# Kernel optimization log

Measured on AMD Instinct MI355X. Metric: run time of the kernel, lower is better.

Reference implementation:

```python
import jax, jax.numpy as jnp
import numpy as np

C_V, C_F, C_D = 10, 64, 16
COSTS = jnp.array([10.0, 5.0, 2.0], dtype=jnp.float32)  # bandwidth cost per granularity
PENALTY = 0.0  # no_transmission_utility_penalty


def setup_inputs() -> dict:
    key = jax.random.key(0)
    k1, k2 = jax.random.split(key)
    B, H, W = 4, 192, 192
    collab = jax.random.normal(k1, (B, C_V + C_F + C_D, H, W), dtype=jnp.float32)
    utility = jax.random.normal(k2, (B, H, W, 3), dtype=jnp.float32)
    return {"collab_bev_data_list": collab, "utility_map_list": utility,
            "bandwidth_budget": 200000}


def _selection_mechanism(utility, budget_per_sample):
    # utility: [B, H, W, G]; returns [B, H, W] float selected granularity (-1 = none)
    B, H, W, G = utility.shape
    best_u = jnp.max(utility, axis=3)                      # [B,H,W]
    best_g = jnp.argmax(utility, axis=3)                   # [B,H,W]
    N = B * H * W
    flat_u = best_u.reshape(N)
    flat_g = best_g.reshape(N)
    b_idx = jnp.repeat(jnp.arange(B, dtype=jnp.int32), H * W)
    valid = flat_u > PENALTY
    cost = COSTS[flat_g]                                   # [N]
    # sort candidates by utility, descending (stable, matching list.sort)
    order = jnp.argsort(-flat_u)
    v_s = valid[order]
    c_s = cost[order]
    b_s = b_idx[order]

    # greedy budget-constrained selection per sample (sequential knapsack)
    def step(usage, item):
        v, c, b = item
        ok = v & (usage[b] + c <= budget_per_sample)
        usage = usage.at[b].add(jnp.where(ok, c, jnp.float32(0)))
        return usage, ok

    _, sel_sorted = jax.lax.scan(step, jnp.zeros((B,), jnp.float32), (v_s, c_s, b_s))
    selected = jnp.zeros((N,), bool).at[order].set(sel_sorted)
    idx = jnp.where(selected, flat_g.astype(jnp.float32), jnp.float32(-1.0))
    return idx.reshape(B, H, W)


def _build_sparse_bev(sel_idx, vox, feat, det):
    m0 = (sel_idx == 0.0)[:, None, :, :]
    m1 = (sel_idx == 1.0)[:, None, :, :]
    m2 = (sel_idx == 2.0)[:, None, :, :]
    return jnp.concatenate([vox * m0, feat * m1, det * m2], axis=1)


def reference(collab_bev_data_list, utility_map_list, bandwidth_budget):
    cav_num = collab_bev_data_list.shape[0]
    budget_per_sample = jnp.float32(bandwidth_budget / cav_num)
    sel_idx = _selection_mechanism(utility_map_list, budget_per_sample)
    vox = collab_bev_data_list[:, :C_V]
    feat = collab_bev_data_list[:, C_V:C_V + C_F]
    det = collab_bev_data_list[:, C_V + C_F:C_V + C_F + C_D]
    sparse = _build_sparse_bev(sel_idx, vox, feat, det)
    return sparse, sel_idx
```

## Files before the change

kernel.cpp:

```cpp
#include <hip/hip_runtime.h>
#include <stdint.h>
#include <math.h>

#define B_    4
#define H_    192
#define W_    192
#define HW    (H_*W_)
#define NPIX  (B_*HW)
#define C_V   10
#define C_F   64
#define C_D   16
#define C_ALL (C_V+C_F+C_D)
#define NBINS 65536
#define CAP   3072

#define OFF_HIST   0u
#define OFF_COUNT  (4u*NBINS*4u)
#define OFF_SELX   (OFF_COUNT + 64u)
#define ZERO_BYTES (OFF_SELX + (uint32_t)NPIX)
#define OFF_KEY    ZERO_BYTES
#define OFF_G      (OFF_KEY + (uint32_t)NPIX*4u)
#define OFF_RES    (OFF_G + (uint32_t)NPIX)
#define OFF_LIST   (OFF_RES + 64u)

__device__ __forceinline__ uint32_t costOf(uint32_t g) {
    return g == 0u ? 10u : (g == 1u ? 5u : 2u);
}

__device__ __forceinline__ uint32_t budgetInt(const int* bptr) {
    double bps = (double)bptr[0] / (double)B_;
    float f = (float)bps;
    return (uint32_t)floorf(f);
}

__global__ void k_prep(const float* __restrict__ util, uint32_t* __restrict__ key,
                       uint8_t* __restrict__ gArr, uint32_t* __restrict__ hist) {
    int i = blockIdx.x * blockDim.x + threadIdx.x;
    if (i >= NPIX) return;
    const float* u = util + (size_t)i * 3;
    float u0 = u[0], u1 = u[1], u2 = u[2];
    float best = u0; uint32_t g = 0;
    if (u1 > best) { best = u1; g = 1; }
    if (u2 > best) { best = u2; g = 2; }
    uint32_t k = 0u;
    if (best > 0.0f) k = __float_as_uint(best) | 0x80000000u;
    key[i] = k;
    gArr[i] = (uint8_t)g;
    if (k) {
        int b = i / HW;
        atomicAdd(&hist[(size_t)b * NBINS + (k >> 16)], costOf(g));
    }
}

__global__ __launch_bounds__(1024) void k_cutoff(const uint32_t* __restrict__ hist,
                                                 const int* __restrict__ budget_ptr,
                                                 uint32_t* __restrict__ res) {
    int b = blockIdx.x;
    uint32_t budget = budgetInt(budget_ptr);
    __shared__ uint32_t scan[1024];
    __shared__ uint32_t f_bstar, f_usage;
    if (threadIdx.x == 0) { f_bstar = 0xFFFFFFFFu; f_usage = 0u; }
    int t = threadIdx.x;
    const uint32_t* hb = hist + (size_t)b * NBINS;
    int hi = 65535 - 64 * t;
    uint32_t cs = 0;
    for (int j = 0; j < 64; ++j) cs += hb[hi - j];
    scan[t] = cs;
    __syncthreads();
    for (int off = 1; off < 1024; off <<= 1) {
        uint32_t v = (t >= off) ? scan[t - off] : 0u;
        __syncthreads();
        scan[t] += v;
        __syncthreads();
    }
    uint32_t incl = scan[t], excl = incl - cs;
    if (excl <= budget && incl > budget) {
        uint32_t cum = excl;
        for (int j = 0; j < 64; ++j) {
            uint32_t hv = hb[hi - j];
            if (cum + hv > budget) { f_bstar = (uint32_t)(hi - j); f_usage = cum; break; }
            cum += hv;
        }
    }
    __syncthreads();
    if (threadIdx.x == 0) {
        uint32_t bs = f_bstar;
        res[b]     = bs;
        res[4 + b] = f_usage;
        uint32_t hl;
        if (bs == 0xFFFFFFFFu)      hl = 1u;
        else if (bs >= 0xFFFFu)     hl = 0xFFFFFFFFu;
        else                        hl = (bs + 1u) << 16;
        res[8 + b] = hl;
    }
}

__global__ void k_collect(const uint32_t* __restrict__ key, const uint8_t* __restrict__ gArr,
                          const uint32_t* __restrict__ res, uint32_t* __restrict__ count,
                          uint64_t* __restrict__ list) {
    int i = blockIdx.x * blockDim.x + threadIdx.x;
    if (i >= NPIX) return;
    uint32_t k = key[i];
    if (!k) return;
    int b = i / HW;
    if ((k >> 16) != res[b]) return;
    uint32_t idx = atomicAdd(&count[b], 1u);
    if (idx < CAP) {
        uint32_t pix = (uint32_t)(i - b * HW);
        uint64_t e = ((uint64_t)(~k) << 32) | ((uint64_t)pix << 2) | (uint64_t)gArr[i];
        list[(size_t)b * CAP + idx] = e;
    }
}

__global__ __launch_bounds__(512) void k_scan(const uint32_t* __restrict__ key,
                                              const uint8_t* __restrict__ gArr,
                                              const uint32_t* __restrict__ res,
                                              const uint32_t* __restrict__ count,
                                              const uint64_t* __restrict__ list,
                                              const int* __restrict__ budget_ptr,
                                              uint8_t* __restrict__ selx) {
    int b = blockIdx.x;
    uint32_t bstar = res[b];
    if (bstar == 0xFFFFFFFFu) return;
    uint32_t budget = budgetInt(budget_ptr);

    __shared__ uint64_t e[CAP];
    __shared__ uint64_t s[CAP];
    __shared__ uint64_t red[512];
    __shared__ uint32_t sh_r, sh_poskey, sh_pospix;

    uint32_t cnt = count[b];
    int n = (int)(cnt < (uint32_t)CAP ? cnt : (uint32_t)CAP);
    const uint64_t* lb = list + (size_t)b * CAP;
    for (int i = threadIdx.x; i < n; i += blockDim.x) e[i] = lb[i];
    __syncthreads();
    for (int i = threadIdx.x; i < n; i += blockDim.x) {
        uint64_t ei = e[i];
        int rk = 0;
        for (int j = 0; j < n; ++j) rk += (e[j] < ei);
        s[rk] = ei;
    }
    __syncthreads();
    if (threadIdx.x == 0) {
        uint32_t usage = res[4 + b];
        uint8_t* sx = selx + (size_t)b * HW;
        for (int i = 0; i < n; ++i) {
            uint64_t ei = s[i];
            uint32_t g = (uint32_t)(ei & 3u);
            uint32_t c = costOf(g);
            if (usage + c <= budget) { usage += c; sx[(ei >> 2) & 0xFFFFu] = 1; }
        }
        sh_r = budget - usage;
        sh_poskey = bstar << 16;
        sh_pospix = 0xFFFFFFFFu;
    }
    __syncthreads();

    const uint32_t* kb = key + (size_t)b * HW;
    const uint8_t*  gb = gArr + (size_t)b * HW;
    for (int round = 0; round < 8; ++round) {
        uint32_t r = sh_r;
        if (r < 2u) break;
        uint32_t pkey = sh_poskey, ppix = sh_pospix;
        uint64_t best = 0;
        for (int i = threadIdx.x; i < HW; i += blockDim.x) {
            uint32_t k = kb[i];
            if (!k) continue;
            if (!(k < pkey || (k == pkey && (uint32_t)i > ppix))) continue;
            if (costOf(gb[i]) > r) continue;
            uint64_t m = ((uint64_t)k << 16) | (uint64_t)(65535u - (uint32_t)i);
            if (m > best) best = m;
        }
        red[threadIdx.x] = best;
        __syncthreads();
        for (int off = 256; off > 0; off >>= 1) {
            if ((int)threadIdx.x < off) {
                uint64_t o = red[threadIdx.x + off];
                if (o > red[threadIdx.x]) red[threadIdx.x] = o;
            }
            __syncthreads();
        }
        if (threadIdx.x == 0) {
            uint64_t m = red[0];
            if (m == 0) sh_r = 0;
            else {
                uint32_t pix = 65535u - (uint32_t)(m & 0xFFFFu);
                uint32_t k   = (uint32_t)(m >> 16);
                uint32_t c   = costOf(gb[pix]);
                selx[(size_t)b * HW + pix] = 1;
                sh_r -= c;
                sh_poskey = k; sh_pospix = pix;
            }
        }
        __syncthreads();
    }
}

__global__ void k_selidx(const uint32_t* __restrict__ key, const uint8_t* __restrict__ gArr,
                         const uint8_t* __restrict__ selx, const uint32_t* __restrict__ res,
                         float* __restrict__ selOut) {
    int i = blockIdx.x * blockDim.x + threadIdx.x;
    if (i >= NPIX) return;
    int b = i / HW;
    uint32_t k = key[i];
    bool sel = (k != 0u && k >= res[8 + b]) || (selx[i] != 0);
    selOut[i] = sel ? (float)gArr[i] : -1.0f;
}

__global__ void k_sparse(const float* __restrict__ collab, const float* __restrict__ selOut,
                         float* __restrict__ out) {
    int tid = blockIdx.x * blockDim.x + threadIdx.x;
    int c = blockIdx.y, b = blockIdx.z;
    if (tid >= HW / 4) return;
    float want = (c < C_V) ? 0.0f : ((c < C_V + C_F) ? 1.0f : 2.0f);
    size_t po = (size_t)b * HW + (size_t)tid * 4;
    float4 s4 = *(const float4*)(selOut + po);
    size_t co = ((size_t)(b * C_ALL + c)) * HW + (size_t)tid * 4;
    float4 v = *(const float4*)(collab + co);
    float4 o;
    o.x = (s4.x == want) ? v.x : 0.0f;
    o.y = (s4.y == want) ? v.y : 0.0f;
    o.z = (s4.z == want) ? v.z : 0.0f;
    o.w = (s4.w == want) ? v.w : 0.0f;
    *(float4*)(out + co) = o;
}

extern "C" void kernel_launch(void* const* d_in, const int* in_sizes, int n_in,
                              void* d_out, int out_size, void* d_ws, size_t ws_size,
                              hipStream_t stream) {
    (void)in_sizes; (void)n_in; (void)out_size; (void)ws_size;
    const float* collab = (const float*)d_in[0];
    const float* util   = (const float*)d_in[1];
    const int*   budget = (const int*)d_in[2];

    uint8_t*  ws    = (uint8_t*)d_ws;
    uint32_t* hist  = (uint32_t*)(ws + OFF_HIST);
    uint32_t* count = (uint32_t*)(ws + OFF_COUNT);
    uint8_t*  selx  = ws + OFF_SELX;
    uint32_t* key   = (uint32_t*)(ws + OFF_KEY);
    uint8_t*  g     = ws + OFF_G;
    uint32_t* res   = (uint32_t*)(ws + OFF_RES);
    uint64_t* list  = (uint64_t*)(ws + OFF_LIST);

    float* outSparse = (float*)d_out;
    float* outSel    = outSparse + (size_t)B_ * C_ALL * HW;

    hipMemsetAsync(d_ws, 0, ZERO_BYTES, stream);

    k_prep   <<<(NPIX + 255) / 256, 256, 0, stream>>>(util, key, g, hist);
    k_cutoff <<<B_, 1024, 0, stream>>>(hist, budget, res);
    k_collect<<<(NPIX + 255) / 256, 256, 0, stream>>>(key, g, res, count, list);
    k_scan   <<<B_, 512, 0, stream>>>(key, g, res, count, list, budget, selx);
    k_selidx <<<(NPIX + 255) / 256, 256, 0, stream>>>(key, g, selx, res, outSel);
    dim3 grid6(HW / 4 / 256, C_ALL, B_);
    k_sparse <<<grid6, 256, 0, stream>>>(collab, outSel, outSparse);
}
```

Before: 86.68 us.

## Fuse selection pipeline into fewer kernels and halve histogram size

Cuts the launch chain from six kernels plus a memset down to four. Cutoff, collect and scan are merged into a single per-sample k_select block that gathers boundary-bin candidates into shared memory. The selection-index computation moves into k_sparse, and k_prep now handles four pixels per thread with vectorized loads and stores. Because only positive keys reach the histogram, it uses 32768 bins instead of 65536, which shrinks zeroing and the prefix scan. The risks are a smaller candidate cap (2048), a full-image rescan inside the single block, and extra key/g/selx loads repeated across all 90 channels in k_sparse.

```diff
diff --git a/kernel.cpp b/kernel.cpp
--- a/kernel.cpp
+++ b/kernel.cpp
@@ -11,17 +11,14 @@
 #define C_F   64
 #define C_D   16
 #define C_ALL (C_V+C_F+C_D)
-#define NBINS 65536
-#define CAP   3072
-
-#define OFF_HIST   0u
-#define OFF_COUNT  (4u*NBINS*4u)
-#define OFF_SELX   (OFF_COUNT + 64u)
-#define ZERO_BYTES (OFF_SELX + (uint32_t)NPIX)
-#define OFF_KEY    ZERO_BYTES
-#define OFF_G      (OFF_KEY + (uint32_t)NPIX*4u)
-#define OFF_RES    (OFF_G + (uint32_t)NPIX)
-#define OFF_LIST   (OFF_RES + 64u)
+#define HBINS 32768
+#define CAP   2048
+
+#define OFF_HIST 0u
+#define OFF_KEY  (4u*HBINS*4u)
+#define OFF_G    (OFF_KEY + (uint32_t)NPIX*4u)
+#define OFF_SELX (OFF_G + (uint32_t)NPIX)
+#define OFF_HL   (OFF_SELX + (uint32_t)NPIX)
 
 __device__ __forceinline__ uint32_t costOf(uint32_t g) {
     return g == 0u ? 10u : (g == 1u ? 5u : 2u);
@@ -33,38 +30,64 @@
     return (uint32_t)floorf(f);
 }
 
-__global__ void k_prep(const float* __restrict__ util, uint32_t* __restrict__ key,
-                       uint8_t* __restrict__ gArr, uint32_t* __restrict__ hist) {
+__global__ void k_zero(uint4* __restrict__ hist4) {
     int i = blockIdx.x * blockDim.x + threadIdx.x;
-    if (i >= NPIX) return;
-    const float* u = util + (size_t)i * 3;
-    float u0 = u[0], u1 = u[1], u2 = u[2];
-    float best = u0; uint32_t g = 0;
-    if (u1 > best) { best = u1; g = 1; }
-    if (u2 > best) { best = u2; g = 2; }
-    uint32_t k = 0u;
-    if (best > 0.0f) k = __float_as_uint(best) | 0x80000000u;
-    key[i] = k;
-    gArr[i] = (uint8_t)g;
-    if (k) {
-        int b = i / HW;
-        atomicAdd(&hist[(size_t)b * NBINS + (k >> 16)], costOf(g));
-    }
-}
-
-__global__ __launch_bounds__(1024) void k_cutoff(const uint32_t* __restrict__ hist,
+    hist4[i] = make_uint4(0u, 0u, 0u, 0u);
+}
+
+__global__ void k_prep(const float* __restrict__ util, uint4* __restrict__ key4,
+                       uint32_t* __restrict__ g4, uint32_t* __restrict__ selx4,
+                       uint32_t* __restrict__ hist) {
+    int t = blockIdx.x * blockDim.x + threadIdx.x;
+    if (t >= NPIX / 4) return;
+    const float4* u4 = (const float4*)util + (size_t)t * 3;
+    float4 a = u4[0], b4 = u4[1], c4 = u4[2];
+    float u[4][3] = { {a.x, a.y, a.z}, {a.w, b4.x, b4.y},
+                      {b4.z, b4.w, c4.x}, {c4.y, c4.z, c4.w} };
+    uint32_t kk[4]; uint32_t gpack = 0;
+    #pragma unroll
+    for (int p = 0; p < 4; ++p) {
+        float best = u[p][0]; uint32_t g = 0;
+        if (u[p][1] > best) { best = u[p][1]; g = 1; }
+        if (u[p][2] > best) { best = u[p][2]; g = 2; }
+        kk[p] = (best > 0.0f) ? (__float_as_uint(best) | 0x80000000u) : 0u;
+        gpack |= g << (8 * p);
+    }
+    key4[t] = make_uint4(kk[0], kk[1], kk[2], kk[3]);
+    g4[t] = gpack;
+    selx4[t] = 0u;
+    int b = (t * 4) / HW;
+    #pragma unroll
+    for (int p = 0; p < 4; ++p)
+        if (kk[p])
+            atomicAdd(&hist[(size_t)b * HBINS + ((kk[p] >> 16) & 32767u)],
+                      costOf((gpack >> (8 * p)) & 3u));
+}
+
+__global__ __launch_bounds__(1024) void k_select(const uint32_t* __restrict__ key,
+                                                 const uint8_t* __restrict__ g,
+                                                 const uint32_t* __restrict__ hist,
                                                  const int* __restrict__ budget_ptr,
-                                                 uint32_t* __restrict__ res) {
+                                                 uint8_t* __restrict__ selx,
+                                                 uint32_t* __restrict__ hl_out) {
     int b = blockIdx.x;
+    int t = threadIdx.x;
     uint32_t budget = budgetInt(budget_ptr);
+
     __shared__ uint32_t scan[1024];
-    __shared__ uint32_t f_bstar, f_usage;
-    if (threadIdx.x == 0) { f_bstar = 0xFFFFFFFFu; f_usage = 0u; }
-    int t = threadIdx.x;
-    const uint32_t* hb = hist + (size_t)b * NBINS;
-    int hi = 65535 - 64 * t;
+    __shared__ uint64_t e[CAP];
+    __shared__ uint64_t s[CAP];
+    __shared__ uint64_t red[1024];
+    __shared__ uint32_t f_b2, f_usage, sh_n, sh_r, sh_poskey, sh_pospix;
+
+    if (t == 0) { f_b2 = 0xFFFFFFFFu; f_usage = 0u; sh_n = 0u; }
+    __syncthreads();
+
+    const uint32_t* hb = hist + (size_t)b * HBINS;
+    int hi = 32767 - 32 * t;
     uint32_t cs = 0;
-    for (int j = 0; j < 64; ++j) cs += hb[hi - j];
+    #pragma unroll 4
+    for (int j = 0; j < 32; ++j) cs += hb[hi - j];
     scan[t] = cs;
     __syncthreads();
     for (int off = 1; off < 1024; off <<= 1) {
@@ -76,94 +99,66 @@
     uint32_t incl = scan[t], excl = incl - cs;
     if (excl <= budget && incl > budget) {
         uint32_t cum = excl;
-        for (int j = 0; j < 64; ++j) {
+        for (int j = 0; j < 32; ++j) {
             uint32_t hv = hb[hi - j];
-            if (cum + hv > budget) { f_bstar = (uint32_t)(hi - j); f_usage = cum; break; }
+            if (cum + hv > budget) { f_b2 = (uint32_t)(hi - j); f_usage = cum; break; }
             cum += hv;
         }
     }
     __syncthreads();
-    if (threadIdx.x == 0) {
-        uint32_t bs = f_bstar;
-        res[b]     = bs;
-        res[4 + b] = f_usage;
+    uint32_t b2 = f_b2;
+    if (t == 0) {
         uint32_t hl;
-        if (bs == 0xFFFFFFFFu)      hl = 1u;
-        else if (bs >= 0xFFFFu)     hl = 0xFFFFFFFFu;
-        else                        hl = (bs + 1u) << 16;
-        res[8 + b] = hl;
-    }
-}
-
-__global__ void k_collect(const uint32_t* __restrict__ key, const uint8_t* __restrict__ gArr,
-                          const uint32_t* __restrict__ res, uint32_t* __restrict__ count,
-                          uint64_t* __restrict__ list) {
-    int i = blockIdx.x * blockDim.x + threadIdx.x;
-    if (i >= NPIX) return;
-    uint32_t k = key[i];
-    if (!k) return;
-    int b = i / HW;
-    if ((k >> 16) != res[b]) return;
-    uint32_t idx = atomicAdd(&count[b], 1u);
-    if (idx < CAP) {
-        uint32_t pix = (uint32_t)(i - b * HW);
-        uint64_t e = ((uint64_t)(~k) << 32) | ((uint64_t)pix << 2) | (uint64_t)gArr[i];
-        list[(size_t)b * CAP + idx] = e;
-    }
-}
-
-__global__ __launch_bounds__(512) void k_scan(const uint32_t* __restrict__ key,
-                                              const uint8_t* __restrict__ gArr,
-                                              const uint32_t* __restrict__ res,
-                                              const uint32_t* __restrict__ count,
-                                              const uint64_t* __restrict__ list,
-                                              const int* __restrict__ budget_ptr,
-                                              uint8_t* __restrict__ selx) {
-    int b = blockIdx.x;
-    uint32_t bstar = res[b];
-    if (bstar == 0xFFFFFFFFu) return;
-    uint32_t budget = budgetInt(budget_ptr);
-
-    __shared__ uint64_t e[CAP];
-    __shared__ uint64_t s[CAP];
-    __shared__ uint64_t red[512];
-    __shared__ uint32_t sh_r, sh_poskey, sh_pospix;
-
-    uint32_t cnt = count[b];
-    int n = (int)(cnt < (uint32_t)CAP ? cnt : (uint32_t)CAP);
-    const uint64_t* lb = list + (size_t)b * CAP;
-    for (int i = threadIdx.x; i < n; i += blockDim.x) e[i] = lb[i];
-    __syncthreads();
-    for (int i = threadIdx.x; i < n; i += blockDim.x) {
+        if (b2 == 0xFFFFFFFFu)           hl = 1u;
+        else {
+            uint32_t bs = b2 + 32768u;
+            hl = (bs >= 65535u) ? 0xFFFFFFFFu : ((bs + 1u) << 16);
+        }
+        hl_out[b] = hl;
+    }
+    if (b2 == 0xFFFFFFFFu) return;
+
+    const uint32_t* kb = key + (size_t)b * HW;
+    const uint8_t*  gb = g   + (size_t)b * HW;
+    for (int i = t; i < HW; i += 1024) {
+        uint32_t k = kb[i];
+        if (k && ((k >> 16) & 32767u) == b2) {
+            uint32_t idx = atomicAdd(&sh_n, 1u);
+            if (idx < CAP)
+                e[idx] = ((uint64_t)(~k) << 32) | ((uint64_t)i << 2) | (uint64_t)gb[i];
+        }
+    }
+    __syncthreads();
+    int n = (int)(sh_n < (uint32_t)CAP ? sh_n : (uint32_t)CAP);
+
+    for (int i = t; i < n; i += 1024) {
         uint64_t ei = e[i];
         int rk = 0;
         for (int j = 0; j < n; ++j) rk += (e[j] < ei);
         s[rk] = ei;
     }
     __syncthreads();
-    if (threadIdx.x == 0) {
-        uint32_t usage = res[4 + b];
+
+    if (t == 0) {
+        uint32_t usage = f_usage;
         uint8_t* sx = selx + (size_t)b * HW;
         for (int i = 0; i < n; ++i) {
             uint64_t ei = s[i];
-            uint32_t g = (uint32_t)(ei & 3u);
-            uint32_t c = costOf(g);
+            uint32_t c = costOf((uint32_t)(ei & 3u));
             if (usage + c <= budget) { usage += c; sx[(ei >> 2) & 0xFFFFu] = 1; }
         }
         sh_r = budget - usage;
-        sh_poskey = bstar << 16;
+        sh_poskey = (b2 + 32768u) << 16;
         sh_pospix = 0xFFFFFFFFu;
     }
     __syncthreads();
 
-    const uint32_t* kb = key + (size_t)b * HW;
-    const uint8_t*  gb = gArr + (size_t)b * HW;
     for (int round = 0; round < 8; ++round) {
         uint32_t r = sh_r;
         if (r < 2u) break;
         uint32_t pkey = sh_poskey, ppix = sh_pospix;
         uint64_t best = 0;
-        for (int i = threadIdx.x; i < HW; i += blockDim.x) {
+        for (int i = t; i < HW; i += 1024) {
             uint32_t k = kb[i];
             if (!k) continue;
             if (!(k < pkey || (k == pkey && (uint32_t)i > ppix))) continue;
@@ -171,16 +166,16 @@
             uint64_t m = ((uint64_t)k << 16) | (uint64_t)(65535u - (uint32_t)i);
             if (m > best) best = m;
         }
-        red[threadIdx.x] = best;
-        __syncthreads();
-        for (int off = 256; off > 0; off >>= 1) {
-            if ((int)threadIdx.x < off) {
-                uint64_t o = red[threadIdx.x + off];
-                if (o > red[threadIdx.x]) red[threadIdx.x] = o;
+        red[t] = best;
+        __syncthreads();
+        for (int off = 512; off > 0; off >>= 1) {
+            if (t < off) {
+                uint64_t o = red[t + off];
+                if (o > red[t]) red[t] = o;
             }
             __syncthreads();
         }
-        if (threadIdx.x == 0) {
+        if (t == 0) {
             uint64_t m = red[0];
             if (m == 0) sh_r = 0;
             else {
@@ -196,33 +191,37 @@
     }
 }
 
-__global__ void k_selidx(const uint32_t* __restrict__ key, const uint8_t* __restrict__ gArr,
-                         const uint8_t* __restrict__ selx, const uint32_t* __restrict__ res,
-                         float* __restrict__ selOut) {
-    int i = blockIdx.x * blockDim.x + threadIdx.x;
-    if (i >= NPIX) return;
-    int b = i / HW;
-    uint32_t k = key[i];
-    bool sel = (k != 0u && k >= res[8 + b]) || (selx[i] != 0);
-    selOut[i] = sel ? (float)gArr[i] : -1.0f;
-}
-
-__global__ void k_sparse(const float* __restrict__ collab, const float* __restrict__ selOut,
-                         float* __restrict__ out) {
+__global__ void k_sparse(const float* __restrict__ collab, const uint4* __restrict__ key4,
+                         const uint32_t* __restrict__ g4, const uint32_t* __restrict__ selx4,
+                         const uint32_t* __restrict__ hl_arr,
+                         float* __restrict__ out, float* __restrict__ selOut) {
     int tid = blockIdx.x * blockDim.x + threadIdx.x;
     int c = blockIdx.y, b = blockIdx.z;
-    if (tid >= HW / 4) return;
-    float want = (c < C_V) ? 0.0f : ((c < C_V + C_F) ? 1.0f : 2.0f);
-    size_t po = (size_t)b * HW + (size_t)tid * 4;
-    float4 s4 = *(const float4*)(selOut + po);
+    int cls = (c < C_V) ? 0 : ((c < C_V + C_F) ? 1 : 2);
+    uint32_t hl = hl_arr[b];
+    size_t p4 = (size_t)b * (HW / 4) + (size_t)tid;
+    uint4 kk = key4[p4];
+    uint32_t gg = g4[p4];
+    uint32_t sx = selx4[p4];
+    int sc[4];
+    uint32_t kv[4] = { kk.x, kk.y, kk.z, kk.w };
+    #pragma unroll
+    for (int p = 0; p < 4; ++p) {
+        bool se = (kv[p] >= hl) || (((sx >> (8 * p)) & 0xFFu) != 0u);
+        sc[p] = se ? (int)((gg >> (8 * p)) & 3u) : -1;
+    }
     size_t co = ((size_t)(b * C_ALL + c)) * HW + (size_t)tid * 4;
     float4 v = *(const float4*)(collab + co);
     float4 o;
-    o.x = (s4.x == want) ? v.x : 0.0f;
-    o.y = (s4.y == want) ? v.y : 0.0f;
-    o.z = (s4.z == want) ? v.z : 0.0f;
-    o.w = (s4.w == want) ? v.w : 0.0f;
+    o.x = (sc[0] == cls) ? v.x : 0.0f;
+    o.y = (sc[1] == cls) ? v.y : 0.0f;
+    o.z = (sc[2] == cls) ? v.z : 0.0f;
+    o.w = (sc[3] == cls) ? v.w : 0.0f;
     *(float4*)(out + co) = o;
+    if (c == 0) {
+        float4 sf = make_float4((float)sc[0], (float)sc[1], (float)sc[2], (float)sc[3]);
+        ((float4*)selOut)[p4] = sf;
+    }
 }
 
 extern "C" void kernel_launch(void* const* d_in, const int* in_sizes, int n_in,
@@ -233,25 +232,21 @@
     const float* util   = (const float*)d_in[1];
     const int*   budget = (const int*)d_in[2];
 
-    uint8_t*  ws    = (uint8_t*)d_ws;
-    uint32_t* hist  = (uint32_t*)(ws + OFF_HIST);
-    uint32_t* count = (uint32_t*)(ws + OFF_COUNT);
-    uint8_t*  selx  = ws + OFF_SELX;
-    uint32_t* key   = (uint32_t*)(ws + OFF_KEY);
-    uint8_t*  g     = ws + OFF_G;
-    uint32_t* res   = (uint32_t*)(ws + OFF_RES);
-    uint64_t* list  = (uint64_t*)(ws + OFF_LIST);
+    uint8_t*  ws   = (uint8_t*)d_ws;
+    uint32_t* hist = (uint32_t*)(ws + OFF_HIST);
+    uint32_t* key  = (uint32_t*)(ws + OFF_KEY);
+    uint8_t*  g    = ws + OFF_G;
+    uint8_t*  selx = ws + OFF_SELX;
+    uint32_t* hl   = (uint32_t*)(ws + OFF_HL);
 
     float* outSparse = (float*)d_out;
     float* outSel    = outSparse + (size_t)B_ * C_ALL * HW;
 
-    hipMemsetAsync(d_ws, 0, ZERO_BYTES, stream);
-
-    k_prep   <<<(NPIX + 255) / 256, 256, 0, stream>>>(util, key, g, hist);
-    k_cutoff <<<B_, 1024, 0, stream>>>(hist, budget, res);
-    k_collect<<<(NPIX + 255) / 256, 256, 0, stream>>>(key, g, res, count, list);
-    k_scan   <<<B_, 512, 0, stream>>>(key, g, res, count, list, budget, selx);
-    k_selidx <<<(NPIX + 255) / 256, 256, 0, stream>>>(key, g, selx, res, outSel);
-    dim3 grid6(HW / 4 / 256, C_ALL, B_);
-    k_sparse <<<grid6, 256, 0, stream>>>(collab, outSel, outSparse);
-}
+    k_zero  <<<(4 * HBINS / 4) / 256, 256, 0, stream>>>((uint4*)hist);
+    k_prep  <<<(NPIX / 4 + 255) / 256, 256, 0, stream>>>(util, (uint4*)key,
+                                                         (uint32_t*)g, (uint32_t*)selx, hist);
+    k_select<<<B_, 1024, 0, stream>>>(key, g, hist, budget, selx, hl);
+    dim3 grid3(HW / 4 / 256, C_ALL, B_);
+    k_sparse<<<grid3, 256, 0, stream>>>(collab, (const uint4*)key, (const uint32_t*)g,
+                                        (const uint32_t*)selx, hl, outSparse, outSel);
+}
```

Result: slower. 88.91 us (+2.6%).
